# Optimization experiments

Hardware: AMD Instinct MI355X
Metric: run time of the kernel (lower is better)

Reference implementation:

```python
import jax, jax.numpy as jnp
import numpy as np

N_NODES = 50000
N_EDGES = 800000
D_NODE = 128      # n_in_node_props
D_EDGE = 32       # n_in_edge_props
L_EDGE = 16       # n_latent_edges
L_NODE = 64       # n_latent_nodes
D_OUT = 128       # n_out_node_props


def setup_inputs() -> dict:
    key = jax.random.key(0)
    ks = jax.random.split(key, 8)
    x = jax.random.normal(ks[0], (N_NODES, D_NODE), dtype=jnp.float32)
    edge_index = jax.random.randint(ks[1], (2, N_EDGES), 0, N_NODES, dtype=jnp.int64)
    edge_attr = jax.random.normal(ks[2], (N_EDGES, D_EDGE), dtype=jnp.float32)
    W_gcn = jax.random.normal(ks[3], (D_NODE, L_NODE), dtype=jnp.float32) * (1.0 / np.sqrt(D_NODE))
    b_gcn = jnp.zeros((L_NODE,), dtype=jnp.float32)
    W_edge = jax.random.normal(ks[4], (D_EDGE, L_EDGE), dtype=jnp.float32) * (1.0 / np.sqrt(D_EDGE))
    b_edge = jnp.zeros((L_EDGE,), dtype=jnp.float32)
    W_node = jax.random.normal(ks[5], (L_EDGE * L_NODE, D_OUT), dtype=jnp.float32) * (1.0 / np.sqrt(L_EDGE * L_NODE))
    b_node = jnp.zeros((D_OUT,), dtype=jnp.float32)
    return {"x": x, "edge_index": edge_index, "edge_attr": edge_attr,
            "W_gcn": W_gcn, "b_gcn": b_gcn, "W_edge": W_edge, "b_edge": b_edge,
            "W_node": W_node, "b_node": b_node}


def reference(x, edge_index, edge_attr, W_gcn, b_gcn, W_edge, b_edge, W_node, b_node):
    """LatentGraph forward: per-latent-channel GCNConv (with self-loops and
    symmetric normalization, PyG semantics) followed by an MLP over the
    concatenated channel outputs."""
    N = x.shape[0]
    # edge latent weights: [E, L], ReLU ensures non-negative edge weights
    edge_props = jax.nn.relu(edge_attr @ W_edge + b_edge)
    # shared GCN linear transform of node features: [N, C]
    xW = x @ W_gcn
    # add self loops (weight 1) once; reused by every channel
    loop = jnp.arange(N)
    row = jnp.concatenate([edge_index[0], loop])  # source (message origin)
    col = jnp.concatenate([edge_index[1], loop])  # target (aggregation)

    def one_channel(carry, w):  # w: [E] latent edge weights for this channel
        wf = jnp.concatenate([w, jnp.ones((N,), w.dtype)])  # [E+N]
        deg = jax.ops.segment_sum(wf, col, num_segments=N)  # weighted in-degree
        dinv = jnp.where(deg > 0, jax.lax.rsqrt(deg), 0.0)
        norm = dinv[row] * wf * dinv[col]                   # [E+N]
        out = jax.ops.segment_sum(norm[:, None] * xW[row], col, num_segments=N)
        return carry, out + b_gcn                            # [N, C]

    _, outs = jax.lax.scan(one_channel, None, edge_props.T)  # [L, N, C]
    # concat over channels in loop order -> [N, L*C]
    feats = jnp.transpose(outs, (1, 0, 2)).reshape(N, L_EDGE * L_NODE)
    return jax.nn.relu(feats @ W_node + b_node)  # y: [N, D_OUT]
```

## Files before the change

### kernel.cpp

```cpp
#include <hip/hip_runtime.h>
#include <hip/hip_fp16.h>

typedef _Float16 f16x8 __attribute__((ext_vector_type(8)));
typedef float f32x4 __attribute__((ext_vector_type(4)));
typedef unsigned u32x4 __attribute__((ext_vector_type(4)));
typedef unsigned short u16;

#define DN 128
#define DE 32
#define LE 16
#define LN 64
#define DOUT 128

__device__ inline u16 f2h(float f) { return __half_as_ushort(__float2half(f)); }
__device__ inline float h2f(u16 u) { return __half2float(__ushort_as_half(u)); }
__device__ inline unsigned pack2h(float lo, float hi) {
  return (unsigned)f2h(lo) | ((unsigned)f2h(hi) << 16);
}
__device__ inline void unp2(unsigned u, float& a, float& b) {
  __half2 p = *reinterpret_cast<__half2*>(&u);
  a = __half2float(__low2half(p));
  b = __half2float(__high2half(p));
}
__device__ inline __half2 u2h2(unsigned u) {
  return *reinterpret_cast<__half2*>(&u);
}
__device__ inline unsigned h22u(__half2 h) {
  return *reinterpret_cast<unsigned*>(&h);
}
__device__ inline unsigned hmulu(u16 a, u16 b) {
  return (unsigned)__half_as_ushort(__hmul(__ushort_as_half(a), __ushort_as_half(b)));
}

__device__ inline void packb_one(const float* __restrict__ W, u16* __restrict__ Bp,
                                 int idx, int K, int NCOL) {
  int KT = K >> 5;
  int lane = idx & 63;
  int rest = idx >> 6;
  int kt = rest % KT, nt = rest / KT;
  int col = nt * 16 + (lane & 15);
  int kb = kt * 32 + (lane >> 4) * 8;
  u16* dst = Bp + (size_t)idx * 8;
#pragma unroll
  for (int i = 0; i < 8; ++i) dst[i] = f2h(W[(size_t)(kb + i) * NCOL + col]);
}

__global__ __launch_bounds__(256) void k_count(const int* __restrict__ ei,
    int* __restrict__ cnt, int* __restrict__ rank, int E) {
  int e = blockIdx.x * 256 + threadIdx.x;
  if (e < E) rank[e] = atomicAdd(&cnt[ei[E + e]], 1);
}

__global__ __launch_bounds__(1024) void k_scan_packb(const int* __restrict__ cnt,
    int* __restrict__ offs, int N,
    const float* __restrict__ Wg, u16* __restrict__ WgP,
    const float* __restrict__ Wn, u16* __restrict__ WnP) {
  const int totA = (DN / 32) * (LN / 16) * 64;
  const int totB = ((LE * LN) / 32) * (DOUT / 16) * 64;
  if (blockIdx.x != 0) {
    int idx = (blockIdx.x - 1) * 1024 + threadIdx.x;
    if (idx < totA) packb_one(Wg, WgP, idx, DN, LN);
    else if (idx < totA + totB) packb_one(Wn, WnP, idx - totA, LE * LN, DOUT);
    return;
  }
  __shared__ int wsum[16];
  int t = threadIdx.x;
  int chunk = (N + 1023) >> 10;
  int s0 = t * chunk;
  int s1 = min(s0 + chunk, N);
  int s = 0;
  for (int i = s0; i < s1; ++i) s += cnt[i];
  int lane = t & 63, wid = t >> 6;
  int v = s;
#pragma unroll
  for (int d = 1; d < 64; d <<= 1) {
    int u = __shfl_up(v, d);
    if (lane >= d) v += u;
  }
  if (lane == 63) wsum[wid] = v;
  __syncthreads();
  if (t == 0) {
    int run = 0;
    for (int w = 0; w < 16; ++w) { int xv = wsum[w]; wsum[w] = run; run += xv; }
  }
  __syncthreads();
  int run = v - s + wsum[wid];
  for (int i = s0; i < s1; ++i) { offs[i] = run; run += cnt[i]; }
  if (s1 == N && s0 < N) offs[N] = run;
}

__global__ __launch_bounds__(256) void k_fill_mlp(const float* __restrict__ ea,
    const float* __restrict__ We, const float* __restrict__ be,
    const int* __restrict__ ei, const int* __restrict__ rank,
    const int* __restrict__ offs,
    int* __restrict__ src, u16* __restrict__ wh, int E) {
  int e = blockIdx.x * 256 + threadIdx.x;
  if (e >= E) return;
  const float4* a4 = (const float4*)(ea + (size_t)e * DE);
  float a[DE];
#pragma unroll
  for (int j = 0; j < DE / 4; ++j) {
    float4 v = a4[j];
    a[4*j] = v.x; a[4*j+1] = v.y; a[4*j+2] = v.z; a[4*j+3] = v.w;
  }
  float acc[LE];
#pragma unroll
  for (int l = 0; l < LE; ++l) acc[l] = be[l];
#pragma unroll
  for (int k = 0; k < DE; ++k) {
    float av = a[k];
#pragma unroll
    for (int l = 0; l < LE; ++l) acc[l] = fmaf(av, We[k * LE + l], acc[l]);
  }
  uint4 o0, o1;
  o0.x = pack2h(fmaxf(acc[0], 0.f), fmaxf(acc[1], 0.f));
  o0.y = pack2h(fmaxf(acc[2], 0.f), fmaxf(acc[3], 0.f));
  o0.z = pack2h(fmaxf(acc[4], 0.f), fmaxf(acc[5], 0.f));
  o0.w = pack2h(fmaxf(acc[6], 0.f), fmaxf(acc[7], 0.f));
  o1.x = pack2h(fmaxf(acc[8], 0.f), fmaxf(acc[9], 0.f));
  o1.y = pack2h(fmaxf(acc[10], 0.f), fmaxf(acc[11], 0.f));
  o1.z = pack2h(fmaxf(acc[12], 0.f), fmaxf(acc[13], 0.f));
  o1.w = pack2h(fmaxf(acc[14], 0.f), fmaxf(acc[15], 0.f));
  int c = ei[E + e];
  int pos = offs[c] + rank[e];
  src[pos] = ei[e];
  uint4* o4 = (uint4*)(wh + (size_t)pos * LE);
  o4[0] = o0; o4[1] = o1;
}

template <int K, int NCOL, int MT, bool FIN, bool AF32, bool OUT16>
__device__ inline void gemm_body(int bid, const void* __restrict__ Av,
    const u16* __restrict__ Bp, const float* __restrict__ bias,
    void* __restrict__ outv, int M) {
  constexpr int NT = NCOL / 16;
  constexpr int KT = K / 32;
  const u16* A16 = (const u16*)Av;
  const float* A32 = (const float*)Av;
  int lane = threadIdx.x & 63;
  int wid = threadIdx.x >> 6;
  int m0 = bid * (MT * 64) + wid * (MT * 16);
  f32x4 acc[MT][NT];
#pragma unroll
  for (int mt = 0; mt < MT; ++mt)
#pragma unroll
    for (int nt = 0; nt < NT; ++nt) {
      acc[mt][nt][0] = 0.f; acc[mt][nt][1] = 0.f;
      acc[mt][nt][2] = 0.f; acc[mt][nt][3] = 0.f;
    }
  int rr[MT]; bool vv[MT];
#pragma unroll
  for (int mt = 0; mt < MT; ++mt) {
    rr[mt] = m0 + mt * 16 + (lane & 15);
    vv[mt] = rr[mt] < M;
  }
  int ko = (lane >> 4) * 8;
#pragma unroll 8
  for (int kt = 0; kt < KT; ++kt) {
    f16x8 a[MT];
#pragma unroll
    for (int mt = 0; mt < MT; ++mt) {
#pragma unroll
      for (int i = 0; i < 8; ++i) a[mt][i] = (_Float16)0.f;
      if constexpr (AF32) {
        if (vv[mt]) {
          const float4* p4 = (const float4*)(A32 + (size_t)rr[mt] * K + ko + kt * 32);
          float4 u0 = p4[0], u1 = p4[1];
          a[mt][0]=(_Float16)u0.x; a[mt][1]=(_Float16)u0.y;
          a[mt][2]=(_Float16)u0.z; a[mt][3]=(_Float16)u0.w;
          a[mt][4]=(_Float16)u1.x; a[mt][5]=(_Float16)u1.y;
          a[mt][6]=(_Float16)u1.z; a[mt][7]=(_Float16)u1.w;
        }
      } else {
        if (vv[mt]) a[mt] = *(const f16x8*)(A16 + (size_t)rr[mt] * K + ko + kt * 32);
      }
    }
#pragma unroll
    for (int nt = 0; nt < NT; ++nt) {
      f16x8 b = *(const f16x8*)(Bp + ((size_t)(nt * KT + kt) * 64 + lane) * 8);
#pragma unroll
      for (int mt = 0; mt < MT; ++mt)
        acc[mt][nt] = __builtin_amdgcn_mfma_f32_16x16x32_f16(a[mt], b, acc[mt][nt], 0, 0, 0);
    }
  }
  int col0 = lane & 15;
#pragma unroll
  for (int mt = 0; mt < MT; ++mt) {
    int rb = m0 + mt * 16 + ((lane >> 4) << 2);
#pragma unroll
    for (int nt = 0; nt < NT; ++nt) {
      int c = nt * 16 + col0;
      float bb = FIN ? bias[c] : 0.f;
#pragma unroll
      for (int r = 0; r < 4; ++r) {
        int row = rb + r;
        if (row < M) {
          float vvv = acc[mt][nt][r] + bb;
          if (FIN) vvv = fmaxf(vvv, 0.f);
          if constexpr (OUT16) ((u16*)outv)[(size_t)row * NCOL + c] = f2h(vvv);
          else ((float*)outv)[(size_t)row * NCOL + c] = vvv;
        }
      }
    }
  }
}

__global__ __launch_bounds__(256) void k_dinv_gemm1(const u16* __restrict__ wh,
    const int* __restrict__ offs, u16* __restrict__ dinvh, int N, int DB,
    const float* __restrict__ x, const u16* __restrict__ WgP, u16* __restrict__ xwh) {
  if ((int)blockIdx.x >= DB) {
    gemm_body<DN, LN, 1, false, true, true>(blockIdx.x - DB, x, WgP, nullptr, xwh, N);
    return;
  }
  int t = threadIdx.x;
  int n = blockIdx.x * 16 + (t >> 4);
  int l = t & 15;
  if (n >= N) return;
  int i0 = offs[n], i1 = offs[n + 1];
  float s = 1.0f;
  for (int i = i0; i < i1; ++i) s += h2f(wh[(size_t)i * LE + l]);
  dinvh[(size_t)n * LE + l] = f2h(rsqrtf(s));
}

__device__ inline void feats_epilogue(int n, int l, int colb, const __half2* acc,
    const u16* __restrict__ dinvh, const u16* __restrict__ xwh,
    const float* __restrict__ bgcn, u16* __restrict__ feats) {
  float dn = h2f(dinvh[(size_t)n * LE + l]);
  float dn2 = dn * dn;
  const u32x4* xs4 = (const u32x4*)(xwh + (size_t)n * LN + colb);
  u32x4 m0 = xs4[0], m1 = xs4[1];
  const f32x4* bgp = (const f32x4*)(bgcn + colb);
  f32x4 b0 = bgp[0], b1 = bgp[1], b2 = bgp[2], b3 = bgp[3];
  float xv[16];
  unp2(m0[0], xv[0], xv[1]);   unp2(m0[1], xv[2], xv[3]);
  unp2(m0[2], xv[4], xv[5]);   unp2(m0[3], xv[6], xv[7]);
  unp2(m1[0], xv[8], xv[9]);   unp2(m1[1], xv[10], xv[11]);
  unp2(m1[2], xv[12], xv[13]); unp2(m1[3], xv[14], xv[15]);
  float av[16];
  unp2(h22u(acc[0]), av[0], av[1]);   unp2(h22u(acc[1]), av[2], av[3]);
  unp2(h22u(acc[2]), av[4], av[5]);   unp2(h22u(acc[3]), av[6], av[7]);
  unp2(h22u(acc[4]), av[8], av[9]);   unp2(h22u(acc[5]), av[10], av[11]);
  unp2(h22u(acc[6]), av[12], av[13]); unp2(h22u(acc[7]), av[14], av[15]);
  float bgv[16] = {b0[0],b0[1],b0[2],b0[3],b1[0],b1[1],b1[2],b1[3],
                   b2[0],b2[1],b2[2],b2[3],b3[0],b3[1],b3[2],b3[3]};
  float ov[16];
#pragma unroll
  for (int j = 0; j < 16; ++j) ov[j] = bgv[j] + dn * av[j] + dn2 * xv[j];
  u32x4 o0, o1;
  o0[0] = pack2h(ov[0], ov[1]);   o0[1] = pack2h(ov[2], ov[3]);
  o0[2] = pack2h(ov[4], ov[5]);   o0[3] = pack2h(ov[6], ov[7]);
  o1[0] = pack2h(ov[8], ov[9]);   o1[1] = pack2h(ov[10], ov[11]);
  o1[2] = pack2h(ov[12], ov[13]); o1[3] = pack2h(ov[14], ov[15]);
  u32x4* ob = (u32x4*)(feats + (size_t)n * (LE * LN) + l * LN + colb);
  ob[0] = o0; ob[1] = o1;
}

__global__ __launch_bounds__(256) void k_feats11(const int* __restrict__ src,
    const u16* __restrict__ wh, const u16* __restrict__ dinvh,
    const u16* __restrict__ xwh, const float* __restrict__ bgcn,
    const int* __restrict__ offs, u16* __restrict__ feats, int N) {
  int wid = threadIdx.x >> 6;
  int n0 = blockIdx.x * 8 + wid * 2;
  if (n0 >= N) return;
  int n1 = n0 + 1;
  bool v1 = n1 < N;
  int lane = threadIdx.x & 63;
  int l = lane & 15, g = lane >> 4;
  int colb = g * 16;
  const u16* xb = xwh + colb;
  __half2 accA[8], accB[8];
#pragma unroll
  for (int j = 0; j < 8; ++j) { accA[j] = u2h2(0u); accB[j] = u2h2(0u); }
  int iA = offs[n0], eA = offs[n0 + 1];
  int iB = v1 ? offs[n1] : 0;
  int eB = v1 ? offs[n1 + 1] : 0;
  int sA = (iA < eA) ? src[iA] : 0;
  int sB = (iB < eB) ? src[iB] : 0;
  while (iA < eA || iB < eB) {
    bool aA = iA < eA, aB = iB < eB;
    u16 wA = 0, dA = 0, wB = 0, dB = 0;
    u32x4 rA0 = {0,0,0,0}, rA1 = {0,0,0,0}, rB0 = {0,0,0,0}, rB1 = {0,0,0,0};
    int sAn = sA, sBn = sB;
    if (aA) {
      wA = wh[(size_t)iA * LE + l];
      dA = dinvh[(size_t)sA * LE + l];
      const u32x4* q = (const u32x4*)(xb + (size_t)sA * LN);
      rA0 = q[0]; rA1 = q[1];
      if (iA + 1 < eA) sAn = src[iA + 1];
    }
    if (aB) {
      wB = wh[(size_t)iB * LE + l];
      dB = dinvh[(size_t)sB * LE + l];
      const u32x4* q = (const u32x4*)(xb + (size_t)sB * LN);
      rB0 = q[0]; rB1 = q[1];
      if (iB + 1 < eB) sBn = src[iB + 1];
    }
    unsigned cAu = hmulu(wA, dA);
    unsigned cBu = hmulu(wB, dB);
    __half2 ca = u2h2(cAu | (cAu << 16));
    __half2 cb = u2h2(cBu | (cBu << 16));
    accA[0] = __hfma2(ca, u2h2(rA0[0]), accA[0]);
    accA[1] = __hfma2(ca, u2h2(rA0[1]), accA[1]);
    accA[2] = __hfma2(ca, u2h2(rA0[2]), accA[2]);
    accA[3] = __hfma2(ca, u2h2(rA0[3]), accA[3]);
    accA[4] = __hfma2(ca, u2h2(rA1[0]), accA[4]);
    accA[5] = __hfma2(ca, u2h2(rA1[1]), accA[5]);
    accA[6] = __hfma2(ca, u2h2(rA1[2]), accA[6]);
    accA[7] = __hfma2(ca, u2h2(rA1[3]), accA[7]);
    accB[0] = __hfma2(cb, u2h2(rB0[0]), accB[0]);
    accB[1] = __hfma2(cb, u2h2(rB0[1]), accB[1]);
    accB[2] = __hfma2(cb, u2h2(rB0[2]), accB[2]);
    accB[3] = __hfma2(cb, u2h2(rB0[3]), accB[3]);
    accB[4] = __hfma2(cb, u2h2(rB1[0]), accB[4]);
    accB[5] = __hfma2(cb, u2h2(rB1[1]), accB[5]);
    accB[6] = __hfma2(cb, u2h2(rB1[2]), accB[6]);
    accB[7] = __hfma2(cb, u2h2(rB1[3]), accB[7]);
    sA = sAn; sB = sBn;
    iA += aA ? 1 : 0;
    iB += aB ? 1 : 0;
  }
  feats_epilogue(n0, l, colb, accA, dinvh, xwh, bgcn, feats);
  if (v1) feats_epilogue(n1, l, colb, accB, dinvh, xwh, bgcn, feats);
}

template <int K, int NCOL, int MT, bool FIN, bool AF32, bool OUT16>
__global__ __launch_bounds__(256) void k_gemm(const void* __restrict__ Av,
    const u16* __restrict__ Bp, const float* __restrict__ bias,
    void* __restrict__ outv, int M) {
  gemm_body<K, NCOL, MT, FIN, AF32, OUT16>(blockIdx.x, Av, Bp, bias, outv, M);
}

extern "C" void kernel_launch(void* const* d_in, const int* in_sizes, int n_in,
                              void* d_out, int out_size, void* d_ws, size_t ws_size,
                              hipStream_t stream) {
  const float* x  = (const float*)d_in[0];
  const int*   ei = (const int*)d_in[1];
  const float* ea = (const float*)d_in[2];
  const float* Wg = (const float*)d_in[3];
  const float* bg = (const float*)d_in[4];
  const float* We = (const float*)d_in[5];
  const float* be = (const float*)d_in[6];
  const float* Wn = (const float*)d_in[7];
  const float* bn = (const float*)d_in[8];
  float* outp = (float*)d_out;
  int N = in_sizes[0] / DN;
  int E = in_sizes[1] / 2;

  char* p = (char*)d_ws;
  auto carve = [&](size_t bytes) {
    char* r = p;
    p += (bytes + 255) & ~(size_t)255;
    return (void*)r;
  };
  u16*   wh    = (u16*)carve((size_t)E * LE * 2);
  u16*   xwh   = (u16*)carve((size_t)N * LN * 2);
  u16*   feats = (u16*)carve((size_t)N * (LE * LN) * 2);
  u16*   dinvh = (u16*)carve((size_t)N * LE * 2);
  u16*   WnP   = (u16*)carve((size_t)(LE * LN) * DOUT * 2);
  u16*   WgP   = (u16*)carve((size_t)DN * LN * 2);
  int*   offs  = (int*)carve((size_t)(N + 1) * 4);
  int*   cnt   = (int*)carve((size_t)N * 4);
  int*   rank  = (int*)carve((size_t)E * 4);
  int*   src   = (int*)carve((size_t)E * 4);

  hipMemsetAsync(cnt, 0, (size_t)N * 4, stream);

  k_count<<<(E + 255) / 256, 256, 0, stream>>>(ei, cnt, rank, E);
  k_scan_packb<<<18, 1024, 0, stream>>>(cnt, offs, N, Wg, WgP, Wn, WnP);
  k_fill_mlp<<<(E + 255) / 256, 256, 0, stream>>>(ea, We, be, ei, rank, offs, src, wh, E);
  int DB = (N + 15) / 16, GB = (N + 63) / 64;
  k_dinv_gemm1<<<DB + GB, 256, 0, stream>>>(wh, offs, dinvh, N, DB, x, WgP, xwh);
  k_feats11<<<(N + 7) / 8, 256, 0, stream>>>(src, wh, dinvh, xwh, bg, offs, feats, N);
  k_gemm<LE * LN, DOUT, 1, true, false, false><<<(N + 63) / 64, 256, 0, stream>>>(feats, WnP, bn, outp, N);
}
```

Before: 349.7 us.

## Fuse feature aggregation with final MLP GEMM via swizzled LDS tile

Merges the per-node GCN aggregation kernel and the final node MLP GEMM into one kernel. Each 512-thread block aggregates 16 nodes into a swizzled shared-memory tile and then runs MFMA over K=1024 against the packed W_node, applying bias and ReLU. This removes the global write and re-read of the N x 1024 fp16 feature matrix and one kernel launch. In exchange, every block re-reads the full W_node from cache, the GEMM tile is only 16 rows, and the LDS footprint (about 33 KB per block) limits occupancy.

```diff
diff --git a/kernel.cpp b/kernel.cpp
--- a/kernel.cpp
+++ b/kernel.cpp
@@ -11,6 +11,7 @@
 #define LE 16
 #define LN 64
 #define DOUT 128
+#define ST 1032
 
 __device__ inline u16 f2h(float f) { return __half_as_ushort(__float2half(f)); }
 __device__ inline float h2f(u16 u) { return __half2float(__ushort_as_half(u)); }
@@ -221,9 +222,9 @@
   dinvh[(size_t)n * LE + l] = f2h(rsqrtf(s));
 }
 
-__device__ inline void feats_epilogue(int n, int l, int colb, const __half2* acc,
+__device__ inline void lds_epilogue(int n, int r, int l, int colb, const __half2* acc,
     const u16* __restrict__ dinvh, const u16* __restrict__ xwh,
-    const float* __restrict__ bgcn, u16* __restrict__ feats) {
+    const float* __restrict__ bgcn, u16* __restrict__ S) {
   float dn = h2f(dinvh[(size_t)n * LE + l]);
   float dn2 = dn * dn;
   const u32x4* xs4 = (const u32x4*)(xwh + (size_t)n * LN + colb);
@@ -250,29 +251,33 @@
   o0[2] = pack2h(ov[4], ov[5]);   o0[3] = pack2h(ov[6], ov[7]);
   o1[0] = pack2h(ov[8], ov[9]);   o1[1] = pack2h(ov[10], ov[11]);
   o1[2] = pack2h(ov[12], ov[13]); o1[3] = pack2h(ov[14], ov[15]);
-  u32x4* ob = (u32x4*)(feats + (size_t)n * (LE * LN) + l * LN + colb);
-  ob[0] = o0; ob[1] = o1;
-}
-
-__global__ __launch_bounds__(256) void k_feats11(const int* __restrict__ src,
+  int off = l * 128 + colb * 2;
+  int swz = (l & 7) << 4;
+  char* rowp = (char*)(S + (size_t)r * ST);
+  *(u32x4*)(rowp + (off ^ swz)) = o0;
+  *(u32x4*)(rowp + ((off + 16) ^ swz)) = o1;
+}
+
+__global__ __launch_bounds__(512) void k_mega(const int* __restrict__ src,
     const u16* __restrict__ wh, const u16* __restrict__ dinvh,
     const u16* __restrict__ xwh, const float* __restrict__ bgcn,
-    const int* __restrict__ offs, u16* __restrict__ feats, int N) {
-  int wid = threadIdx.x >> 6;
-  int n0 = blockIdx.x * 8 + wid * 2;
-  if (n0 >= N) return;
-  int n1 = n0 + 1;
-  bool v1 = n1 < N;
-  int lane = threadIdx.x & 63;
+    const int* __restrict__ offs, const u16* __restrict__ WnP,
+    const float* __restrict__ bn, float* __restrict__ y, int N) {
+  __shared__ u16 S[16 * ST];
+  int tid = threadIdx.x;
+  int w = tid >> 6, lane = tid & 63;
   int l = lane & 15, g = lane >> 4;
   int colb = g * 16;
+  int nblk = blockIdx.x * 16;
+  int r0 = w * 2;
+  int n0 = nblk + r0, n1 = n0 + 1;
+  bool v0 = n0 < N, v1 = n1 < N;
   const u16* xb = xwh + colb;
   __half2 accA[8], accB[8];
 #pragma unroll
   for (int j = 0; j < 8; ++j) { accA[j] = u2h2(0u); accB[j] = u2h2(0u); }
-  int iA = offs[n0], eA = offs[n0 + 1];
-  int iB = v1 ? offs[n1] : 0;
-  int eB = v1 ? offs[n1 + 1] : 0;
+  int iA = v0 ? offs[n0] : 0, eA = v0 ? offs[n0 + 1] : 0;
+  int iB = v1 ? offs[n1] : 0, eB = v1 ? offs[n1 + 1] : 0;
   int sA = (iA < eA) ? src[iA] : 0;
   int sB = (iB < eB) ? src[iB] : 0;
   while (iA < eA || iB < eB) {
@@ -318,15 +323,28 @@
     iA += aA ? 1 : 0;
     iB += aB ? 1 : 0;
   }
-  feats_epilogue(n0, l, colb, accA, dinvh, xwh, bgcn, feats);
-  if (v1) feats_epilogue(n1, l, colb, accB, dinvh, xwh, bgcn, feats);
-}
-
-template <int K, int NCOL, int MT, bool FIN, bool AF32, bool OUT16>
-__global__ __launch_bounds__(256) void k_gemm(const void* __restrict__ Av,
-    const u16* __restrict__ Bp, const float* __restrict__ bias,
-    void* __restrict__ outv, int M) {
-  gemm_body<K, NCOL, MT, FIN, AF32, OUT16>(blockIdx.x, Av, Bp, bias, outv, M);
+  if (v0) lds_epilogue(n0, r0, l, colb, accA, dinvh, xwh, bgcn, S);
+  if (v1) lds_epilogue(n1, r0 + 1, l, colb, accB, dinvh, xwh, bgcn, S);
+  __syncthreads();
+  f32x4 acc2;
+  acc2[0] = 0.f; acc2[1] = 0.f; acc2[2] = 0.f; acc2[3] = 0.f;
+  const char* arow = (const char*)(S + (size_t)(lane & 15) * ST);
+#pragma unroll 8
+  for (int kt = 0; kt < 32; ++kt) {
+    int aoff = kt * 64 + g * 16;
+    int key = ((aoff >> 7) & 7) << 4;
+    f16x8 a = *(const f16x8*)(arow + (aoff ^ key));
+    f16x8 b = *(const f16x8*)(WnP + ((size_t)(w * 32 + kt) * 64 + lane) * 8);
+    acc2 = __builtin_amdgcn_mfma_f32_16x16x32_f16(a, b, acc2, 0, 0, 0);
+  }
+  int col = w * 16 + (lane & 15);
+  float bb = bn[col];
+  int rb = (lane >> 4) * 4;
+#pragma unroll
+  for (int r = 0; r < 4; ++r) {
+    int row = nblk + rb + r;
+    if (row < N) y[(size_t)row * DOUT + col] = fmaxf(acc2[r] + bb, 0.f);
+  }
 }
 
 extern "C" void kernel_launch(void* const* d_in, const int* in_sizes, int n_in,
@@ -353,7 +371,6 @@
   };
   u16*   wh    = (u16*)carve((size_t)E * LE * 2);
   u16*   xwh   = (u16*)carve((size_t)N * LN * 2);
-  u16*   feats = (u16*)carve((size_t)N * (LE * LN) * 2);
   u16*   dinvh = (u16*)carve((size_t)N * LE * 2);
   u16*   WnP   = (u16*)carve((size_t)(LE * LN) * DOUT * 2);
   u16*   WgP   = (u16*)carve((size_t)DN * LN * 2);
@@ -369,6 +386,5 @@
   k_fill_mlp<<<(E + 255) / 256, 256, 0, stream>>>(ea, We, be, ei, rank, offs, src, wh, E);
   int DB = (N + 15) / 16, GB = (N + 63) / 64;
   k_dinv_gemm1<<<DB + GB, 256, 0, stream>>>(wh, offs, dinvh, N, DB, x, WgP, xwh);
-  k_feats11<<<(N + 7) / 8, 256, 0, stream>>>(src, wh, dinvh, xwh, bg, offs, feats, N);
-  k_gemm<LE * LN, DOUT, 1, true, false, false><<<(N + 63) / 64, 256, 0, stream>>>(feats, WnP, bn, outp, N);
-}
+  k_mega<<<(N + 15) / 16, 512, 0, stream>>>(src, wh, dinvh, xwh, bg, offs, WnP, bn, outp, N);
+}
```

New measurement: 298.9 us, median of 2. -14.5%, faster.
